# Kernel optimization log

Measured on AMD Instinct MI355X. Metric: run time of the kernel, lower is better.

## Reference

```python
import jax, jax.numpy as jnp
import numpy as np
import math

IN_DIM = 1024
L = 4096
D_MODEL = 512
D_INNER = 1024   # expand=2 * d_model
D_STATE = 16
D_CONV = 4
DT_RANK = 32     # ceil(d_model / 16)
N_LAYERS = 2
RATE = 10


def setup_inputs() -> dict:
    key = jax.random.key(0)
    ks = iter(jax.random.split(key, 32))
    def w(shape, fan_in):
        return jax.random.normal(next(ks), shape, jnp.float32) * (1.0 / math.sqrt(fan_in))
    return {
        "x": jax.random.normal(next(ks), (1, L, IN_DIM), jnp.float32),
        "rate": RATE,
        "fc1_w": w((D_MODEL, IN_DIM), IN_DIM),
        "fc1_b": jnp.zeros((D_MODEL,), jnp.float32),
        "ln_w": jnp.ones((N_LAYERS, D_MODEL), jnp.float32),
        "ln_b": jnp.zeros((N_LAYERS, D_MODEL), jnp.float32),
        "in_proj_w": w((N_LAYERS, 2 * D_INNER, D_MODEL), D_MODEL),
        "conv_w": w((N_LAYERS, D_INNER, D_CONV), D_CONV),
        "conv_b": jnp.zeros((N_LAYERS, D_INNER), jnp.float32),
        "x_proj_w": w((N_LAYERS, DT_RANK + 2 * D_STATE, D_INNER), D_INNER),
        "dt_proj_w": w((N_LAYERS, D_INNER, DT_RANK), DT_RANK),
        "dt_proj_b": jax.random.normal(next(ks), (N_LAYERS, D_INNER), jnp.float32) * 0.1,
        "A_log": jnp.tile(jnp.log(jnp.arange(1, D_STATE + 1, dtype=jnp.float32)), (N_LAYERS, D_INNER, 1)),
        "D_skip": jnp.ones((N_LAYERS, D_INNER), jnp.float32),
        "out_proj_w": w((N_LAYERS, D_MODEL, D_INNER), D_INNER),
        "norm_w": jnp.ones((D_MODEL,), jnp.float32),
        "norm_b": jnp.zeros((D_MODEL,), jnp.float32),
        "attn_w1": w((128, D_MODEL), D_MODEL),
        "attn_b1": jnp.zeros((128,), jnp.float32),
        "attn_w2": w((1, 128), 128),
        "attn_b2": jnp.zeros((1,), jnp.float32),
        "out2048_w": w((2048, D_MODEL), D_MODEL),
        "out2048_b": jnp.zeros((2048,), jnp.float32),
    }


def _layernorm(x, w, b, eps=1e-5):
    mu = x.mean(-1, keepdims=True)
    var = ((x - mu) ** 2).mean(-1, keepdims=True)
    return (x - mu) * jax.lax.rsqrt(var + eps) * w + b


def _causal_conv(x, w, b):
    # depthwise causal conv: x [L, d], w [d, K] -> y[t, d] = sum_k w[d, k] * x[t - (K-1) + k, d]
    K = w.shape[1]
    xp = jnp.pad(x, ((K - 1, 0), (0, 0)))
    y = sum(xp[k:k + x.shape[0]] * w[:, k] for k in range(K))
    return y + b


def _selective_scan(u, dt, A, B, C, Dp, z):
    # u, dt, z: [L, d]; A: [d, n]; B, C: [L, n]; Dp: [d]
    def step(h, inp):
        dt_t, B_t, C_t, u_t = inp
        dA = jnp.exp(dt_t[:, None] * A)                    # [d, n]
        h = dA * h + (dt_t * u_t)[:, None] * B_t[None, :]  # [d, n]
        return h, h @ C_t                                  # y_t: [d]
    h0 = jnp.zeros((u.shape[1], A.shape[1]), u.dtype)
    _, y = jax.lax.scan(step, h0, (dt, B, C, u))
    return (y + u * Dp) * jax.nn.silu(z)


def _srmamba(h, perm, inv, in_w, cw, cb, xw, dtw, dtb, A_log, Dp, ow):
    xz = h @ in_w.T                         # [L, 2*d_inner]
    x, z = jnp.split(xz, 2, axis=-1)
    x, z = x[perm], z[perm]                 # sequence reordering (stride `rate`)
    x = jax.nn.silu(_causal_conv(x, cw, cb))
    dbl = x @ xw.T                          # [L, dt_rank + 2n]
    dt = jax.nn.softplus(dbl[:, :DT_RANK] @ dtw.T + dtb)
    B = dbl[:, DT_RANK:DT_RANK + D_STATE]
    C = dbl[:, DT_RANK + D_STATE:]
    y = _selective_scan(x, dt, -jnp.exp(A_log), B, C, Dp, z)
    return y[inv] @ ow.T                    # restore original order, out_proj


def reference(x, rate, fc1_w, fc1_b, ln_w, ln_b, in_proj_w, conv_w, conv_b, x_proj_w, dt_proj_w, dt_proj_b, A_log, D_skip, out_proj_w, norm_w, norm_b, attn_w1, attn_b1, attn_w2, attn_b2, out2048_w, out2048_b):
    h = jax.nn.relu(x[0] @ fc1_w.T + fc1_b)   # [L, 512]
    Lx = h.shape[0]
    perm = jnp.concatenate([jnp.arange(i, Lx, rate) for i in range(rate)])
    inv = jnp.argsort(perm)
    for l in range(N_LAYERS):
        h = h + _srmamba(_layernorm(h, ln_w[l], ln_b[l]), perm, inv,
                         in_proj_w[l], conv_w[l], conv_b[l], x_proj_w[l],
                         dt_proj_w[l], dt_proj_b[l], A_log[l], D_skip[l], out_proj_w[l])
    h = _layernorm(h, norm_w, norm_b)
    a = jnp.tanh(h @ attn_w1.T + attn_b1) @ attn_w2.T + attn_b2  # [L, 1]
    Aatt = jax.nn.softmax(a[:, 0])                                # [L]
    pooled = Aatt @ h                                             # [512]
    out = pooled @ out2048_w.T + out2048_b                        # [2048]
    return out[None, :], Aatt[None, None, :]
```

## Files before the change

### kernel.cpp

```cpp
#include <hip/hip_runtime.h>
#include <hip/hip_fp16.h>
#include <math.h>

#define L 4096
#define DIN 1024
#define DM 512
#define DI 1024
#define DS 16
#define DTR 32
#define NCH 256
#define CHK 16

typedef _Float16 v8h __attribute__((ext_vector_type(8)));
typedef _Float16 v4h __attribute__((ext_vector_type(4)));
typedef float v4f __attribute__((ext_vector_type(4)));

__global__ __launch_bounds__(256) void f2h_multi_k(
    const int* __restrict__ ratep, int* __restrict__ perm,
    const float* __restrict__ s0, _Float16* __restrict__ d0, int b0,
    const float* __restrict__ s1, _Float16* __restrict__ d1, int b1,
    const float* __restrict__ s2, _Float16* __restrict__ d2, int b2,
    const float* __restrict__ s3, _Float16* __restrict__ d3, int b3,
    const float* __restrict__ s4, _Float16* __restrict__ d4, int b4,
    const float* __restrict__ s5, _Float16* __restrict__ d5, int b5)
{
    int b = blockIdx.x;
    if (b < 16) {
        int p = b * 256 + threadIdx.x;
        int rate = ratep[0];
        int cum = 0;
        for (int g = 0; g < rate; ++g) {
            int sz = (L - g + rate - 1) / rate;
            if (p < cum + sz) { perm[p] = g + rate * (p - cum); return; }
            cum += sz;
        }
        return;
    }
    b -= 16;
    const float* src; _Float16* dst; int lb;
    if (b < b0)                          { src = s0; dst = d0; lb = b; }
    else if (b < b0 + b1)                { src = s1; dst = d1; lb = b - b0; }
    else if (b < b0 + b1 + b2)           { src = s2; dst = d2; lb = b - b0 - b1; }
    else if (b < b0 + b1 + b2 + b3)      { src = s3; dst = d3; lb = b - b0 - b1 - b2; }
    else if (b < b0 + b1 + b2 + b3 + b4) { src = s4; dst = d4; lb = b - b0 - b1 - b2 - b3; }
    else                                 { src = s5; dst = d5; lb = b - b0 - b1 - b2 - b3 - b4; }
    int i = (lb * 256 + threadIdx.x) * 4;
    float4 v = *(const float4*)(src + i);
    _Float16 h4[4] = {(_Float16)v.x, (_Float16)v.y, (_Float16)v.z, (_Float16)v.w};
    *(uint2*)(dst + i) = *(uint2*)h4;
}

template<int ACT, int BNT, int HALF>
__global__ __launch_bounds__(256) void hgemm_nt(
    const _Float16* __restrict__ A, int lda,
    const _Float16* __restrict__ B, int ldb,
    void* __restrict__ Cv, int ldc,
    const float* __restrict__ bias, int K, int accum)
{
    constexpr int MI = (BNT == 128) ? 4 : 2;
    __shared__ _Float16 As[128][72];
    __shared__ _Float16 Bs[BNT][72];
    int tid = threadIdx.x;
    int m0 = blockIdx.y * 128, n0 = blockIdx.x * BNT;
    int lane = tid & 63, wave = tid >> 6;
    int wm, wn;
    if constexpr (BNT == 128) { wm = (wave >> 1) * 64; wn = (wave & 1) * 64; }
    else                      { wm = wave * 32;        wn = 0; }
    int quad = lane >> 4, r16 = lane & 15;
    v4f acc[MI][4] = {};

    int srow = tid >> 1;
    int scol = (tid & 1) * 32;
    const _Float16* Ag = A + (size_t)(m0 + srow) * lda + scol;
    int srowB = (BNT == 128) ? srow : (tid >> 2);
    int scolB = (BNT == 128) ? scol : (tid & 3) * 16;
    const _Float16* Bg = B + (size_t)(n0 + srowB) * ldb + scolB;

    uint4 a0, a1, a2, a3, b0, b1, b2, b3;
    a0 = *(const uint4*)(Ag);      a1 = *(const uint4*)(Ag + 8);
    a2 = *(const uint4*)(Ag + 16); a3 = *(const uint4*)(Ag + 24);
    b0 = *(const uint4*)(Bg);      b1 = *(const uint4*)(Bg + 8);
    if constexpr (BNT == 128) {
        b2 = *(const uint4*)(Bg + 16); b3 = *(const uint4*)(Bg + 24);
    }

    int KS = K / 64;
    for (int ks = 0; ks < KS; ++ks) {
        __syncthreads();
        *(uint4*)&As[srow][scol]      = a0;
        *(uint4*)&As[srow][scol + 8]  = a1;
        *(uint4*)&As[srow][scol + 16] = a2;
        *(uint4*)&As[srow][scol + 24] = a3;
        *(uint4*)&Bs[srowB][scolB]     = b0;
        *(uint4*)&Bs[srowB][scolB + 8] = b1;
        if constexpr (BNT == 128) {
            *(uint4*)&Bs[srowB][scolB + 16] = b2;
            *(uint4*)&Bs[srowB][scolB + 24] = b3;
        }
        __syncthreads();
        if (ks + 1 < KS) {
            int k0 = (ks + 1) * 64;
            a0 = *(const uint4*)(Ag + k0);      a1 = *(const uint4*)(Ag + k0 + 8);
            a2 = *(const uint4*)(Ag + k0 + 16); a3 = *(const uint4*)(Ag + k0 + 24);
            b0 = *(const uint4*)(Bg + k0);      b1 = *(const uint4*)(Bg + k0 + 8);
            if constexpr (BNT == 128) {
                b2 = *(const uint4*)(Bg + k0 + 16); b3 = *(const uint4*)(Bg + k0 + 24);
            }
        }
#pragma unroll
        for (int kk = 0; kk < 2; ++kk) {
            v8h af[MI], bf[4];
#pragma unroll
            for (int i = 0; i < MI; ++i)
                af[i] = *(const v8h*)&As[wm + i * 16 + r16][kk * 32 + quad * 8];
#pragma unroll
            for (int j = 0; j < 4; ++j)
                bf[j] = *(const v8h*)&Bs[wn + j * 16 + r16][kk * 32 + quad * 8];
#pragma unroll
            for (int i = 0; i < MI; ++i)
#pragma unroll
                for (int j = 0; j < 4; ++j)
                    acc[i][j] = __builtin_amdgcn_mfma_f32_16x16x32_f16(
                        af[i], bf[j], acc[i][j], 0, 0, 0);
        }
    }

#pragma unroll
    for (int i = 0; i < MI; ++i) {
#pragma unroll
        for (int j = 0; j < 4; ++j) {
            int col = n0 + wn + j * 16 + r16;
            int rbase = m0 + wm + i * 16 + quad * 4;
            float bv = bias ? bias[col] : 0.f;
#pragma unroll
            for (int r = 0; r < 4; ++r) {
                float v = acc[i][j][r] + bv;
                if (ACT == 1) v = fmaxf(v, 0.f);
                if constexpr (HALF) {
                    ((_Float16*)Cv)[(size_t)(rbase + r) * ldc + col] = (_Float16)v;
                } else {
                    float* p = (float*)Cv + (size_t)(rbase + r) * ldc + col;
                    if (accum) v += *p;
                    *p = v;
                }
            }
        }
    }
}

__global__ __launch_bounds__(256) void hgemm_xproj(
    const _Float16* __restrict__ A,
    const _Float16* __restrict__ B,
    float* __restrict__ C)
{
    __shared__ _Float16 As[128][40];
    __shared__ _Float16 Bs[64][40];
    int tid = threadIdx.x;
    int m0 = blockIdx.y * 128;
    int kb = blockIdx.z * 128;
    int lane = tid & 63, wave = tid >> 6;
    int wm = wave * 32;
    int quad = lane >> 4, r16 = lane & 15;
    v4f acc[2][4] = {};

    int srow = tid >> 1, scol = (tid & 1) * 16;
    const _Float16* Ag = A + (size_t)(m0 + srow) * DI + kb + scol;
    int srowB = tid >> 2, scolB = (tid & 3) * 8;
    const _Float16* Bg = B + (size_t)srowB * DI + kb + scolB;

    uint4 a0 = *(const uint4*)(Ag);
    uint4 a1 = *(const uint4*)(Ag + 8);
    uint4 b0 = *(const uint4*)(Bg);

    for (int ks = 0; ks < 4; ++ks) {
        __syncthreads();
        *(uint4*)&As[srow][scol] = a0;
        *(uint4*)&As[srow][scol + 8] = a1;
        *(uint4*)&Bs[srowB][scolB] = b0;
        __syncthreads();
        if (ks + 1 < 4) {
            int k0 = (ks + 1) * 32;
            a0 = *(const uint4*)(Ag + k0);
            a1 = *(const uint4*)(Ag + k0 + 8);
            b0 = *(const uint4*)(Bg + k0);
        }
        v8h af[2], bf[4];
#pragma unroll
        for (int i = 0; i < 2; ++i)
            af[i] = *(const v8h*)&As[wm + i * 16 + r16][quad * 8];
#pragma unroll
        for (int j = 0; j < 4; ++j)
            bf[j] = *(const v8h*)&Bs[j * 16 + r16][quad * 8];
#pragma unroll
        for (int i = 0; i < 2; ++i)
#pragma unroll
            for (int j = 0; j < 4; ++j)
                acc[i][j] = __builtin_amdgcn_mfma_f32_16x16x32_f16(
                    af[i], bf[j], acc[i][j], 0, 0, 0);
    }
#pragma unroll
    for (int i = 0; i < 2; ++i) {
#pragma unroll
        for (int j = 0; j < 4; ++j) {
            int col = j * 16 + r16;
            int rbase = m0 + wm + i * 16 + quad * 4;
#pragma unroll
            for (int r = 0; r < 4; ++r)
                atomicAdd(&C[(size_t)(rbase + r) * 64 + col], acc[i][j][r]);
        }
    }
}

__global__ __launch_bounds__(256) void hgemm_attn(
    const _Float16* __restrict__ A,
    const _Float16* __restrict__ B,
    const float* __restrict__ b1, const float* __restrict__ w2,
    float* __restrict__ avec)
{
    __shared__ _Float16 As[128][40];
    __shared__ _Float16 Bs[64][40];
    int tid = threadIdx.x;
    int m0 = blockIdx.y * 128, n0 = blockIdx.x * 64;
    int lane = tid & 63, wave = tid >> 6;
    int wm = wave * 32;
    int quad = lane >> 4, r16 = lane & 15;
    v4f acc[2][4] = {};

    int srow = tid >> 1, scol = (tid & 1) * 16;
    const _Float16* Ag = A + (size_t)(m0 + srow) * DM + scol;
    int srowB = tid >> 2, scolB = (tid & 3) * 8;
    const _Float16* Bg = B + (size_t)(n0 + srowB) * DM + scolB;

    uint4 a0 = *(const uint4*)(Ag);
    uint4 a1 = *(const uint4*)(Ag + 8);
    uint4 b0 = *(const uint4*)(Bg);

    for (int ks = 0; ks < DM / 32; ++ks) {
        __syncthreads();
        *(uint4*)&As[srow][scol] = a0;
        *(uint4*)&As[srow][scol + 8] = a1;
        *(uint4*)&Bs[srowB][scolB] = b0;
        __syncthreads();
        if (ks + 1 < DM / 32) {
            int k0 = (ks + 1) * 32;
            a0 = *(const uint4*)(Ag + k0);
            a1 = *(const uint4*)(Ag + k0 + 8);
            b0 = *(const uint4*)(Bg + k0);
        }
        v8h af[2], bf[4];
#pragma unroll
        for (int i = 0; i < 2; ++i)
            af[i] = *(const v8h*)&As[wm + i * 16 + r16][quad * 8];
#pragma unroll
        for (int j = 0; j < 4; ++j)
            bf[j] = *(const v8h*)&Bs[j * 16 + r16][quad * 8];
#pragma unroll
        for (int i = 0; i < 2; ++i)
#pragma unroll
            for (int j = 0; j < 4; ++j)
                acc[i][j] = __builtin_amdgcn_mfma_f32_16x16x32_f16(
                    af[i], bf[j], acc[i][j], 0, 0, 0);
    }

#pragma unroll
    for (int i = 0; i < 2; ++i) {
        float part[4] = {0.f, 0.f, 0.f, 0.f};
#pragma unroll
        for (int j = 0; j < 4; ++j) {
            int col = n0 + j * 16 + r16;
            float bv = b1[col], wv = w2[col];
#pragma unroll
            for (int r = 0; r < 4; ++r)
                part[r] = fmaf(tanhf(acc[i][j][r] + bv), wv, part[r]);
        }
#pragma unroll
        for (int r = 0; r < 4; ++r) {
            part[r] += __shfl_xor(part[r], 1, 64);
            part[r] += __shfl_xor(part[r], 2, 64);
            part[r] += __shfl_xor(part[r], 4, 64);
            part[r] += __shfl_xor(part[r], 8, 64);
        }
        if (r16 == 0) {
            int rbase = m0 + wm + i * 16 + quad * 4;
#pragma unroll
            for (int r = 0; r < 4; ++r)
                atomicAdd(&avec[rbase + r], part[r]);
        }
    }
}

#define BM 64
#define BN 64
#define BKK 32
__global__ __launch_bounds__(256) void gemm_dt(
    const float* __restrict__ A, int lda,
    const float* __restrict__ B, int ldb,
    _Float16* __restrict__ C, int ldc,
    const float* __restrict__ bias, int K)
{
    __shared__ float As[BKK][BM + 4];
    __shared__ float Bs[BKK][BN + 4];
    int tid = threadIdx.x;
    int m0 = blockIdx.y * BM;
    int n0 = blockIdx.x * BN;
    int tx = tid & 15, ty = tid >> 4;
    float acc[4][4] = {};
    int arow = tid >> 3;
    int ak = (tid & 7) * 4;

    for (int k0 = 0; k0 < K; k0 += BKK) {
#pragma unroll
        for (int r = 0; r < 2; ++r) {
            int row = arow + r * 32;
            float4 va = *(const float4*)(A + (size_t)(m0 + row) * lda + k0 + ak);
            As[ak + 0][row] = va.x; As[ak + 1][row] = va.y;
            As[ak + 2][row] = va.z; As[ak + 3][row] = va.w;
            float4 vb = *(const float4*)(B + (size_t)(n0 + row) * ldb + k0 + ak);
            Bs[ak + 0][row] = vb.x; Bs[ak + 1][row] = vb.y;
            Bs[ak + 2][row] = vb.z; Bs[ak + 3][row] = vb.w;
        }
        __syncthreads();
#pragma unroll
        for (int kk = 0; kk < BKK; ++kk) {
            float4 a4 = *(const float4*)&As[kk][ty * 4];
            float4 b4 = *(const float4*)&Bs[kk][tx * 4];
            float a[4] = {a4.x, a4.y, a4.z, a4.w};
            float b[4] = {b4.x, b4.y, b4.z, b4.w};
#pragma unroll
            for (int i = 0; i < 4; ++i)
#pragma unroll
                for (int j = 0; j < 4; ++j)
                    acc[i][j] = fmaf(a[i], b[j], acc[i][j]);
        }
        __syncthreads();
    }

#pragma unroll
    for (int i = 0; i < 4; ++i) {
        int row = m0 + ty * 4 + i;
        int col = n0 + tx * 4;
        _Float16 v4[4];
#pragma unroll
        for (int j = 0; j < 4; ++j) {
            float xv = acc[i][j] + bias[col + j];
            xv = (xv > 20.f) ? xv : log1pf(__expf(xv));
            v4[j] = (_Float16)xv;
        }
        *(uint2*)(C + (size_t)row * ldc + col) = *(uint2*)v4;
    }
}

__global__ __launch_bounds__(256) void layernorm_k(
    const float* __restrict__ x, const float* __restrict__ w,
    const float* __restrict__ b, float* __restrict__ o,
    _Float16* __restrict__ oh, float* __restrict__ avec,
    const float* __restrict__ b2)
{
    int row = blockIdx.x;
    int tid = threadIdx.x;
    const float* xr = x + (size_t)row * DM;
    float v0 = xr[tid], v1 = xr[tid + 256];
    float s = v0 + v1, ss = v0 * v0 + v1 * v1;
    for (int off = 32; off; off >>= 1) {
        s += __shfl_down(s, off, 64);
        ss += __shfl_down(ss, off, 64);
    }
    __shared__ float sm[4], sm2[4];
    int wave = tid >> 6, lane = tid & 63;
    if (lane == 0) { sm[wave] = s; sm2[wave] = ss; }
    __syncthreads();
    float tot = sm[0] + sm[1] + sm[2] + sm[3];
    float tot2 = sm2[0] + sm2[1] + sm2[2] + sm2[3];
    float mu = tot * (1.f / DM);
    float var = tot2 * (1.f / DM) - mu * mu;
    float rs = rsqrtf(var + 1e-5f);
    float y0 = (v0 - mu) * rs * w[tid] + b[tid];
    float y1 = (v1 - mu) * rs * w[tid + 256] + b[tid + 256];
    o[(size_t)row * DM + tid] = y0;
    o[(size_t)row * DM + tid + 256] = y1;
    if (oh) {
        oh[(size_t)row * DM + tid] = (_Float16)y0;
        oh[(size_t)row * DM + tid + 256] = (_Float16)y1;
    }
    if (avec && tid == 0) avec[row] = b2[0];
}

__global__ __launch_bounds__(256) void conv_silu_k(
    const _Float16* __restrict__ xz, const int* __restrict__ perm,
    const float* __restrict__ cw, const float* __restrict__ cb,
    _Float16* __restrict__ xc, float* __restrict__ dbl)
{
    if (blockIdx.x < 256) {
        int zi = (blockIdx.x * 256 + threadIdx.x) * 4;
        *(float4*)(dbl + zi) = make_float4(0.f, 0.f, 0.f, 0.f);
    }
    int g = blockIdx.x * 256 + threadIdx.x;
    int c = g & (DI - 1), p = g >> 10;
    float acc = cb[c];
#pragma unroll
    for (int k = 0; k < 4; ++k) {
        int q = p + k - 3;
        if (q >= 0)
            acc = fmaf((float)xz[(size_t)perm[q] * (2 * DI) + c], cw[c * 4 + k], acc);
    }
    float sig = 1.f / (1.f + __expf(-acc));
    xc[g] = (_Float16)(acc * sig);
}

__global__ __launch_bounds__(256) void scan_pass1(
    const _Float16* __restrict__ dt, const _Float16* __restrict__ u,
    const float* __restrict__ dbl, const float* __restrict__ A_log,
    _Float16* __restrict__ Aprod, _Float16* __restrict__ carry)
{
    int c = blockIdx.x * 256 + threadIdx.x;
    int j = blockIdx.y;
    float Ac[16];
#pragma unroll
    for (int s = 0; s < 16; ++s) Ac[s] = -__expf(A_log[c * DS + s]);
    float ap[16], h[16];
#pragma unroll
    for (int s = 0; s < 16; ++s) { ap[s] = 1.f; h[s] = 0.f; }
    int t0 = j * CHK;
    for (int tt = 0; tt < CHK; ++tt) {
        int t = t0 + tt;
        float dtv = (float)dt[(size_t)t * DI + c];
        float uv  = (float)u[(size_t)t * DI + c];
        v4f Bv[4];
#pragma unroll
        for (int q = 0; q < 4; ++q)
            Bv[q] = *(const v4f*)(dbl + (size_t)t * 64 + DTR + q * 4);
        float du = dtv * uv;
#pragma unroll
        for (int s = 0; s < 16; ++s) {
            float dA = __expf(dtv * Ac[s]);
            h[s] = fmaf(dA, h[s], du * Bv[s >> 2][s & 3]);
            ap[s] *= dA;
        }
    }
    size_t base = ((size_t)j * DI + c) * DS;
#pragma unroll
    for (int q = 0; q < 4; ++q) {
        v4h av = {(_Float16)ap[q*4], (_Float16)ap[q*4+1], (_Float16)ap[q*4+2], (_Float16)ap[q*4+3]};
        v4h hv = {(_Float16)h[q*4], (_Float16)h[q*4+1], (_Float16)h[q*4+2], (_Float16)h[q*4+3]};
        *(v4h*)(Aprod + base + q * 4) = av;
        *(v4h*)(carry + base + q * 4) = hv;
    }
}

__global__ __launch_bounds__(256) void scan_pass2(
    const _Float16* __restrict__ Aprod, const _Float16* __restrict__ carry,
    _Float16* __restrict__ Hin)
{
    int idx = blockIdx.x * 256 + threadIdx.x;
    float H = 0.f;
    Hin[idx] = (_Float16)0.f;
    for (int j = 1; j < NCH; ++j) {
        H = fmaf((float)Aprod[(size_t)(j - 1) * (DI * DS) + idx], H,
                 (float)carry[(size_t)(j - 1) * (DI * DS) + idx]);
        Hin[(size_t)j * (DI * DS) + idx] = (_Float16)H;
    }
}

__global__ __launch_bounds__(256) void scan_pass3(
    const _Float16* __restrict__ dt, const _Float16* __restrict__ u,
    const float* __restrict__ dbl, const _Float16* __restrict__ xz,
    const float* __restrict__ A_log, const float* __restrict__ Dsk,
    const int* __restrict__ perm, const _Float16* __restrict__ Hin,
    _Float16* __restrict__ yo)
{
    int c = blockIdx.x * 256 + threadIdx.x;
    int j = blockIdx.y;
    float Ac[16];
#pragma unroll
    for (int s = 0; s < 16; ++s) Ac[s] = -__expf(A_log[c * DS + s]);
    float Dp = Dsk[c];
    float h[16];
    size_t hbase = ((size_t)j * DI + c) * DS;
#pragma unroll
    for (int q = 0; q < 4; ++q) {
        v4h hv = *(const v4h*)(Hin + hbase + q * 4);
#pragma unroll
        for (int r = 0; r < 4; ++r) h[q * 4 + r] = (float)hv[r];
    }
    int t0 = j * CHK;
    for (int tt = 0; tt < CHK; ++tt) {
        int t = t0 + tt;
        float dtv = (float)dt[(size_t)t * DI + c];
        float uv  = (float)u[(size_t)t * DI + c];
        v4f Bv[4], Cv[4];
#pragma unroll
        for (int q = 0; q < 4; ++q) {
            Bv[q] = *(const v4f*)(dbl + (size_t)t * 64 + DTR + q * 4);
            Cv[q] = *(const v4f*)(dbl + (size_t)t * 64 + DTR + DS + q * 4);
        }
        float du = dtv * uv;
        float y = 0.f;
#pragma unroll
        for (int s = 0; s < 16; ++s) {
            float dA = __expf(dtv * Ac[s]);
            h[s] = fmaf(dA, h[s], du * Bv[s >> 2][s & 3]);
            y = fmaf(h[s], Cv[s >> 2][s & 3], y);
        }
        int tp = perm[t];
        float z = (float)xz[(size_t)tp * (2 * DI) + DI + c];
        float sig = 1.f / (1.f + __expf(-z));
        yo[(size_t)tp * DI + c] = (_Float16)((y + uv * Dp) * (z * sig));
    }
}

__global__ __launch_bounds__(1024) void softmax_k(
    const float* __restrict__ a, float* __restrict__ out,
    float* __restrict__ pooled)
{
    int tid = threadIdx.x;
    if (tid < DM) pooled[tid] = 0.f;
    float v[4];
    float mx = -1e30f;
#pragma unroll
    for (int i = 0; i < 4; ++i) { v[i] = a[tid + i * 1024]; mx = fmaxf(mx, v[i]); }
    __shared__ float sm[16];
    for (int off = 32; off; off >>= 1) mx = fmaxf(mx, __shfl_xor(mx, off, 64));
    int wave = tid >> 6, lane = tid & 63;
    if (lane == 0) sm[wave] = mx;
    __syncthreads();
    if (tid < 16) {
        float m = sm[tid];
        for (int off = 8; off; off >>= 1) m = fmaxf(m, __shfl_xor(m, off, 64));
        sm[tid] = m;
    }
    __syncthreads();
    mx = sm[0];
    float s = 0.f;
#pragma unroll
    for (int i = 0; i < 4; ++i) { v[i] = __expf(v[i] - mx); s += v[i]; }
    for (int off = 32; off; off >>= 1) s += __shfl_xor(s, off, 64);
    __syncthreads();
    if (lane == 0) sm[wave] = s;
    __syncthreads();
    if (tid < 16) {
        float t2 = sm[tid];
        for (int off = 8; off; off >>= 1) t2 += __shfl_xor(t2, off, 64);
        sm[tid] = t2;
    }
    __syncthreads();
    float inv = 1.f / sm[0];
#pragma unroll
    for (int i = 0; i < 4; ++i) out[tid + i * 1024] = v[i] * inv;
}

__global__ __launch_bounds__(512) void pool_k(
    const float* __restrict__ aatt, const float* __restrict__ h,
    float* __restrict__ pooled)
{
    int m = threadIdx.x;
    int t0 = blockIdx.x * 128;
    float acc = 0.f;
    for (int r = 0; r < 128; ++r) {
        int t = t0 + r;
        acc = fmaf(aatt[t], h[(size_t)t * DM + m], acc);
    }
    atomicAdd(&pooled[m], acc);
}

__global__ __launch_bounds__(64) void out2048_k(
    const float* __restrict__ pooled, const float* __restrict__ w,
    const float* __restrict__ b, float* __restrict__ out)
{
    int n = blockIdx.x;
    int lane = threadIdx.x;
    const float* wr = w + (size_t)n * DM;
    float acc = 0.f;
#pragma unroll
    for (int k = 0; k < 8; ++k)
        acc = fmaf(wr[lane + k * 64], pooled[lane + k * 64], acc);
    for (int off = 32; off; off >>= 1) acc += __shfl_xor(acc, off, 64);
    if (lane == 0) out[n] = acc + b[n];
}

extern "C" void kernel_launch(void* const* d_in, const int* in_sizes, int n_in,
                              void* d_out, int out_size, void* d_ws, size_t ws_size,
                              hipStream_t stream) {
    const float* x     = (const float*)d_in[0];
    const int*   rate  = (const int*)d_in[1];
    const float* fc1_w = (const float*)d_in[2];
    const float* fc1_b = (const float*)d_in[3];
    const float* ln_w  = (const float*)d_in[4];
    const float* ln_b  = (const float*)d_in[5];
    const float* ipw   = (const float*)d_in[6];
    const float* cw    = (const float*)d_in[7];
    const float* cb    = (const float*)d_in[8];
    const float* xpw   = (const float*)d_in[9];
    const float* dtw   = (const float*)d_in[10];
    const float* dtpb  = (const float*)d_in[11];
    const float* A_log = (const float*)d_in[12];
    const float* Dsk   = (const float*)d_in[13];
    const float* opw   = (const float*)d_in[14];
    const float* nw    = (const float*)d_in[15];
    const float* nb    = (const float*)d_in[16];
    const float* aw1   = (const float*)d_in[17];
    const float* ab1   = (const float*)d_in[18];
    const float* aw2   = (const float*)d_in[19];
    const float* ab2   = (const float*)d_in[20];
    const float* ow    = (const float*)d_in[21];
    const float* ob    = (const float*)d_in[22];
    float* out = (float*)d_out;

    int* perm = (int*)d_ws;
    float* f = (float*)d_ws + 4096;
    float* h    = f; f += (size_t)L * DM;
    float* hln  = f; f += (size_t)L * DM;
    float* dbl  = f; f += (size_t)L * 64;
    float* avec = f; f += L;
    float* pooled = f; f += DM;
    _Float16* fh = (_Float16*)f;
    _Float16* xh     = fh; fh += (size_t)L * DIN;
    _Float16* hln_h  = fh; fh += (size_t)L * DM;
    _Float16* yo_h   = fh; fh += (size_t)L * DI;
    _Float16* xz_h   = fh; fh += (size_t)L * 2 * DI;
    _Float16* xc_h   = fh; fh += (size_t)L * DI;
    _Float16* dtv_h  = fh; fh += (size_t)L * DI;
    _Float16* Aprod  = fh; fh += (size_t)NCH * DI * DS;
    _Float16* carry  = fh; fh += (size_t)NCH * DI * DS;
    _Float16* Hin    = fh; fh += (size_t)NCH * DI * DS;
    _Float16* fc1w_h = fh; fh += (size_t)DM * DIN;
    _Float16* ipw_h  = fh; fh += (size_t)2 * 2 * DI * DM;
    _Float16* opw_h  = fh; fh += (size_t)2 * DM * DI;
    _Float16* xpw_h  = fh; fh += (size_t)2 * 64 * DI;
    _Float16* aw1_h  = fh; fh += (size_t)128 * DM;

    f2h_multi_k<<<16 + (L * DIN + DM * DIN + 2 * 2 * DI * DM + 2 * DM * DI
                   + 2 * 64 * DI + 128 * DM) / 1024, 256, 0, stream>>>(
        rate, perm,
        x, xh, L * DIN / 1024,
        fc1_w, fc1w_h, DM * DIN / 1024,
        ipw, ipw_h, 2 * 2 * DI * DM / 1024,
        opw, opw_h, 2 * DM * DI / 1024,
        xpw, xpw_h, 2 * 64 * DI / 1024,
        aw1, aw1_h, 128 * DM / 1024);

    hgemm_nt<1, 64, 0><<<dim3(DM / 64, L / 128), 256, 0, stream>>>(
        xh, DIN, fc1w_h, DIN, h, DM, fc1_b, DIN, 0);

    for (int l = 0; l < 2; ++l) {
        layernorm_k<<<L, 256, 0, stream>>>(h, ln_w + l * DM, ln_b + l * DM,
                                           hln, hln_h, nullptr, nullptr);
        hgemm_nt<0, 128, 1><<<dim3(2 * DI / 128, L / 128), 256, 0, stream>>>(
            hln_h, DM, ipw_h + (size_t)l * 2 * DI * DM, DM, xz_h, 2 * DI,
            nullptr, DM, 0);
        conv_silu_k<<<L * DI / 256, 256, 0, stream>>>(
            xz_h, perm, cw + (size_t)l * DI * 4, cb + (size_t)l * DI, xc_h, dbl);
        hgemm_xproj<<<dim3(1, L / 128, 8), 256, 0, stream>>>(
            xc_h, xpw_h + (size_t)l * 64 * DI, dbl);
        gemm_dt<<<dim3(DI / 64, L / 64), 256, 0, stream>>>(
            dbl, 64, dtw + (size_t)l * DI * DTR, DTR, dtv_h, DI,
            dtpb + (size_t)l * DI, DTR);
        scan_pass1<<<dim3(DI / 256, NCH), 256, 0, stream>>>(
            dtv_h, xc_h, dbl, A_log + (size_t)l * DI * DS, Aprod, carry);
        scan_pass2<<<DI * DS / 256, 256, 0, stream>>>(Aprod, carry, Hin);
        scan_pass3<<<dim3(DI / 256, NCH), 256, 0, stream>>>(
            dtv_h, xc_h, dbl, xz_h, A_log + (size_t)l * DI * DS,
            Dsk + (size_t)l * DI, perm, Hin, yo_h);
        hgemm_nt<0, 64, 0><<<dim3(DM / 64, L / 128), 256, 0, stream>>>(
            yo_h, DI, opw_h + (size_t)l * DM * DI, DI, h, DM, nullptr, DI, 1);
    }

    layernorm_k<<<L, 256, 0, stream>>>(h, nw, nb, hln, hln_h, avec, ab2);
    hgemm_attn<<<dim3(2, L / 128), 256, 0, stream>>>(
        hln_h, aw1_h, ab1, aw2, avec);
    softmax_k<<<1, 1024, 0, stream>>>(avec, out + 2048, pooled);
    pool_k<<<32, 512, 0, stream>>>(out + 2048, hln, pooled);
    out2048_k<<<2048, 64, 0, stream>>>(pooled, ow, ob, out);
}
```

Baseline: 504.3 us.

## Fuse softmax into attention GEMM via last-block ticket, pool from fp16

Folds the separate single-block softmax kernel into the tail of hgemm_attn: each block takes a global atomic ticket, and the last of the 64 blocks computes the softmax over avec and zeroes pooled. The fp32 layernorm output buffer is dropped, so the pooling reads the fp16 copy instead. Pooling also runs on 128 blocks instead of 32 for more parallelism. This removes one launch and a large fp32 write and read, at the cost of a serialized tail on one block and slightly lower precision in pooling.

```diff
diff --git a/kernel.cpp b/kernel.cpp
--- a/kernel.cpp
+++ b/kernel.cpp
@@ -16,7 +16,7 @@
 typedef float v4f __attribute__((ext_vector_type(4)));
 
 __global__ __launch_bounds__(256) void f2h_multi_k(
-    const int* __restrict__ ratep, int* __restrict__ perm,
+    const int* __restrict__ ratep, int* __restrict__ perm, int* __restrict__ ticket,
     const float* __restrict__ s0, _Float16* __restrict__ d0, int b0,
     const float* __restrict__ s1, _Float16* __restrict__ d1, int b1,
     const float* __restrict__ s2, _Float16* __restrict__ d2, int b2,
@@ -26,6 +26,7 @@
 {
     int b = blockIdx.x;
     if (b < 16) {
+        if (b == 0 && threadIdx.x == 0) *ticket = 0;
         int p = b * 256 + threadIdx.x;
         int rate = ratep[0];
         int cum = 0;
@@ -215,7 +216,8 @@
     const _Float16* __restrict__ A,
     const _Float16* __restrict__ B,
     const float* __restrict__ b1, const float* __restrict__ w2,
-    float* __restrict__ avec)
+    float* __restrict__ avec, int* __restrict__ ticket,
+    float* __restrict__ aatt, float* __restrict__ pooled)
 {
     __shared__ _Float16 As[128][40];
     __shared__ _Float16 Bs[64][40];
@@ -287,6 +289,36 @@
                 atomicAdd(&avec[rbase + r], part[r]);
         }
     }
+
+    __threadfence();
+    __shared__ int st;
+    if (tid == 0) st = atomicAdd(ticket, 1);
+    __syncthreads();
+    if (st != 63) return;
+    __threadfence();
+    float v[16];
+    float mx = -1e30f;
+#pragma unroll
+    for (int i = 0; i < 16; ++i) { v[i] = avec[tid + i * 256]; mx = fmaxf(mx, v[i]); }
+    for (int off = 32; off; off >>= 1) mx = fmaxf(mx, __shfl_xor(mx, off, 64));
+    __shared__ float sred[4];
+    int wv = tid >> 6, ln2 = tid & 63;
+    if (ln2 == 0) sred[wv] = mx;
+    __syncthreads();
+    mx = fmaxf(fmaxf(sred[0], sred[1]), fmaxf(sred[2], sred[3]));
+    float ssum = 0.f;
+#pragma unroll
+    for (int i = 0; i < 16; ++i) { v[i] = __expf(v[i] - mx); ssum += v[i]; }
+    for (int off = 32; off; off >>= 1) ssum += __shfl_xor(ssum, off, 64);
+    __syncthreads();
+    if (ln2 == 0) sred[wv] = ssum;
+    __syncthreads();
+    ssum = sred[0] + sred[1] + sred[2] + sred[3];
+    float inv = 1.f / ssum;
+#pragma unroll
+    for (int i = 0; i < 16; ++i) aatt[tid + i * 256] = v[i] * inv;
+    pooled[tid] = 0.f;
+    pooled[tid + 256] = 0.f;
 }
 
 #define BM 64
@@ -376,12 +408,12 @@
     float rs = rsqrtf(var + 1e-5f);
     float y0 = (v0 - mu) * rs * w[tid] + b[tid];
     float y1 = (v1 - mu) * rs * w[tid + 256] + b[tid + 256];
-    o[(size_t)row * DM + tid] = y0;
-    o[(size_t)row * DM + tid + 256] = y1;
-    if (oh) {
-        oh[(size_t)row * DM + tid] = (_Float16)y0;
-        oh[(size_t)row * DM + tid + 256] = (_Float16)y1;
-    }
+    if (o) {
+        o[(size_t)row * DM + tid] = y0;
+        o[(size_t)row * DM + tid + 256] = y1;
+    }
+    oh[(size_t)row * DM + tid] = (_Float16)y0;
+    oh[(size_t)row * DM + tid + 256] = (_Float16)y1;
     if (avec && tid == 0) avec[row] = b2[0];
 }
 
@@ -508,56 +540,16 @@
     }
 }
 
-__global__ __launch_bounds__(1024) void softmax_k(
-    const float* __restrict__ a, float* __restrict__ out,
+__global__ __launch_bounds__(512) void pool_k(
+    const float* __restrict__ aatt, const _Float16* __restrict__ hh,
     float* __restrict__ pooled)
 {
-    int tid = threadIdx.x;
-    if (tid < DM) pooled[tid] = 0.f;
-    float v[4];
-    float mx = -1e30f;
-#pragma unroll
-    for (int i = 0; i < 4; ++i) { v[i] = a[tid + i * 1024]; mx = fmaxf(mx, v[i]); }
-    __shared__ float sm[16];
-    for (int off = 32; off; off >>= 1) mx = fmaxf(mx, __shfl_xor(mx, off, 64));
-    int wave = tid >> 6, lane = tid & 63;
-    if (lane == 0) sm[wave] = mx;
-    __syncthreads();
-    if (tid < 16) {
-        float m = sm[tid];
-        for (int off = 8; off; off >>= 1) m = fmaxf(m, __shfl_xor(m, off, 64));
-        sm[tid] = m;
-    }
-    __syncthreads();
-    mx = sm[0];
-    float s = 0.f;
-#pragma unroll
-    for (int i = 0; i < 4; ++i) { v[i] = __expf(v[i] - mx); s += v[i]; }
-    for (int off = 32; off; off >>= 1) s += __shfl_xor(s, off, 64);
-    __syncthreads();
-    if (lane == 0) sm[wave] = s;
-    __syncthreads();
-    if (tid < 16) {
-        float t2 = sm[tid];
-        for (int off = 8; off; off >>= 1) t2 += __shfl_xor(t2, off, 64);
-        sm[tid] = t2;
-    }
-    __syncthreads();
-    float inv = 1.f / sm[0];
-#pragma unroll
-    for (int i = 0; i < 4; ++i) out[tid + i * 1024] = v[i] * inv;
-}
-
-__global__ __launch_bounds__(512) void pool_k(
-    const float* __restrict__ aatt, const float* __restrict__ h,
-    float* __restrict__ pooled)
-{
     int m = threadIdx.x;
-    int t0 = blockIdx.x * 128;
+    int t0 = blockIdx.x * 32;
     float acc = 0.f;
-    for (int r = 0; r < 128; ++r) {
+    for (int r = 0; r < 32; ++r) {
         int t = t0 + r;
-        acc = fmaf(aatt[t], h[(size_t)t * DM + m], acc);
+        acc = fmaf(aatt[t], (float)hh[(size_t)t * DM + m], acc);
     }
     atomicAdd(&pooled[m], acc);
 }
@@ -606,9 +598,9 @@
     float* out = (float*)d_out;
 
     int* perm = (int*)d_ws;
-    float* f = (float*)d_ws + 4096;
+    int* ticket = (int*)d_ws + 4096;
+    float* f = (float*)d_ws + 4096 + 256;
     float* h    = f; f += (size_t)L * DM;
-    float* hln  = f; f += (size_t)L * DM;
     float* dbl  = f; f += (size_t)L * 64;
     float* avec = f; f += L;
     float* pooled = f; f += DM;
@@ -630,7 +622,7 @@
 
     f2h_multi_k<<<16 + (L * DIN + DM * DIN + 2 * 2 * DI * DM + 2 * DM * DI
                    + 2 * 64 * DI + 128 * DM) / 1024, 256, 0, stream>>>(
-        rate, perm,
+        rate, perm, ticket,
         x, xh, L * DIN / 1024,
         fc1_w, fc1w_h, DM * DIN / 1024,
         ipw, ipw_h, 2 * 2 * DI * DM / 1024,
@@ -643,7 +635,7 @@
 
     for (int l = 0; l < 2; ++l) {
         layernorm_k<<<L, 256, 0, stream>>>(h, ln_w + l * DM, ln_b + l * DM,
-                                           hln, hln_h, nullptr, nullptr);
+                                           nullptr, hln_h, nullptr, nullptr);
         hgemm_nt<0, 128, 1><<<dim3(2 * DI / 128, L / 128), 256, 0, stream>>>(
             hln_h, DM, ipw_h + (size_t)l * 2 * DI * DM, DM, xz_h, 2 * DI,
             nullptr, DM, 0);
@@ -664,10 +656,9 @@
             yo_h, DI, opw_h + (size_t)l * DM * DI, DI, h, DM, nullptr, DI, 1);
     }
 
-    layernorm_k<<<L, 256, 0, stream>>>(h, nw, nb, hln, hln_h, avec, ab2);
+    layernorm_k<<<L, 256, 0, stream>>>(h, nw, nb, nullptr, hln_h, avec, ab2);
     hgemm_attn<<<dim3(2, L / 128), 256, 0, stream>>>(
-        hln_h, aw1_h, ab1, aw2, avec);
-    softmax_k<<<1, 1024, 0, stream>>>(avec, out + 2048, pooled);
-    pool_k<<<32, 512, 0, stream>>>(out + 2048, hln, pooled);
+        hln_h, aw1_h, ab1, aw2, avec, ticket, out + 2048, pooled);
+    pool_k<<<128, 512, 0, stream>>>(out + 2048, hln_h, pooled);
     out2048_k<<<2048, 64, 0, stream>>>(pooled, ow, ob, out);
 }
```

Result: no change. 499.4 us (-1.0%).
